# Kernel tuning notes

Hardware: AMD Instinct MI355X
Metric: run time of the kernel (lower is better)

The kernel has to match this reference:

```python
import jax, jax.numpy as jnp
import numpy as np

N, E = 40000, 640000
IN_DIM, EDGE_DIM, HID = 128, 64, 128


def setup_inputs() -> dict:
    key = jax.random.key(0)
    ks = jax.random.split(key, 10)
    x = jax.random.normal(ks[0], (N, IN_DIM), dtype=jnp.float32)
    edge_index = jax.random.randint(ks[1], (2, E), 0, N, dtype=jnp.int64)
    edge_attr = jax.random.normal(ks[2], (E, EDGE_DIM), dtype=jnp.float32)
    # learned params (xavier-ish scaling)
    Wh_w = jax.random.normal(ks[3], (EDGE_DIM, HID), dtype=jnp.float32) / np.sqrt(EDGE_DIM)
    Wh_b = jnp.zeros((HID,), dtype=jnp.float32)
    Wn_w = jax.random.normal(ks[4], (2 * IN_DIM, HID), dtype=jnp.float32) / np.sqrt(2 * IN_DIM)
    Wn_b = jnp.zeros((HID,), dtype=jnp.float32)
    w_e = jax.random.normal(ks[5], (HID, 1), dtype=jnp.float32) / np.sqrt(HID)
    ft_w = jax.random.normal(ks[6], (IN_DIM, IN_DIM), dtype=jnp.float32) / np.sqrt(IN_DIM)
    ft_b = jnp.zeros((IN_DIM,), dtype=jnp.float32)
    return {"x": x, "edge_index": edge_index, "edge_attr": edge_attr,
            "Wh_w": Wh_w, "Wh_b": Wh_b, "Wn_w": Wn_w, "Wn_b": Wn_b,
            "w_e": w_e, "ft_w": ft_w, "ft_b": ft_b}


def reference(x, edge_index, edge_attr, Wh_w, Wh_b, Wn_w, Wn_b, w_e, ft_w, ft_b):
    src, dst = edge_index[0], edge_index[1]
    # gather endpoint features and run edge MLP: relu(W_h(e) + W_n([x_src; x_dst]))
    node_feat = jnp.concatenate([x[src], x[dst]], axis=1)          # [E, 2*in_dim]
    edge_h = edge_attr @ Wh_w + Wh_b                               # [E, hid]
    node_h = node_feat @ Wn_w + Wn_b                               # [E, hid]
    combined = jax.nn.relu(edge_h + node_h)
    scores = (combined @ w_e)[:, 0]                                # [E]
    alpha = jax.nn.softmax(scores, axis=0)                         # softmax over all edges
    # scatter-add weighted dst features into src nodes (same-type branch)
    local = jnp.zeros_like(x).at[src].add(-alpha[:, None] * x[dst])
    out = x + local
    out = out + out @ ft_w + ft_b
    return out
```

## Files before the change

kernel.cpp:

```cpp
#include <hip/hip_runtime.h>
#include <math.h>

#define N_NODES 40000
#define E_EDGES 640000
#define IN_DIM 128
#define EDGE_DIM 64
#define HID 128
#define EB 10000
#define NPART (EB * 4)

typedef unsigned int u32;
typedef unsigned short u16;
typedef __attribute__((ext_vector_type(4))) float f32x4;
typedef __attribute__((ext_vector_type(8))) short bf16x8;

__device__ __forceinline__ float bf_lo(u32 d) { return __uint_as_float(d << 16); }
__device__ __forceinline__ float bf_hi(u32 d) { return __uint_as_float(d & 0xffff0000u); }
__device__ __forceinline__ u16 f2bf(float f) {
    u32 u = __float_as_uint(f);
    return (u16)((u + 0x7fffu + ((u >> 16) & 1u)) >> 16);
}
__device__ __forceinline__ u32 pack_bf(float lo, float hi) {
    return ((u32)f2bf(hi) << 16) | (u32)f2bf(lo);
}


__global__ __launch_bounds__(256) void k_init(const float* __restrict__ x,
                                              u16* __restrict__ xb,
                                              u32* __restrict__ counts) {
    int i = blockIdx.x * 256 + threadIdx.x;
    xb[i] = f2bf(x[i]);
    if (i < N_NODES) counts[i] = 0;
}

__global__ __launch_bounds__(256) void k_trans(const float* __restrict__ Whw,
                                               const float* __restrict__ Wnw,
                                               const float* __restrict__ ftw,
                                               u16* __restrict__ Whtb,
                                               u16* __restrict__ WnAT,
                                               u16* __restrict__ WnBT,
                                               u16* __restrict__ fttb) {
    int i = blockIdx.x * 256 + threadIdx.x;
    if (i < 8192) {
        int h = i >> 6, k = i & 63;
        Whtb[i] = f2bf(Whw[k * HID + h]);
    } else if (i < 24576) {
        int j = i - 8192, h = j >> 7, k = j & 127;
        WnAT[j] = f2bf(Wnw[k * HID + h]);
    } else if (i < 40960) {
        int j = i - 24576, h = j >> 7, k = j & 127;
        WnBT[j] = f2bf(Wnw[(IN_DIM + k) * HID + h]);
    } else {
        int j = i - 40960, h = j >> 7, k = j & 127;
        fttb[j] = f2bf(ftw[k * IN_DIM + h]);
    }
}

__global__ __launch_bounds__(256) void k_proj(const u16* __restrict__ xb,
                                              const u16* __restrict__ WnAT,
                                              const u16* __restrict__ WnBT,
                                              const float* __restrict__ Whb,
                                              const float* __restrict__ Wnb,
                                              u16* __restrict__ P1b,
                                              u16* __restrict__ P2b) {
    const int t = threadIdx.x, w = t >> 6, lane = t & 63;
    const int mrow = lane & 15, quad = lane >> 4;
    const int rowBase = blockIdx.x * 64 + w * 16;

    bf16x8 a[4];
    const u16* ar = xb + (size_t)(rowBase + mrow) * IN_DIM + quad * 8;
#pragma unroll
    for (int ks = 0; ks < 4; ++ks) a[ks] = *(const bf16x8*)(ar + ks * 32);

#pragma unroll
    for (int nt = 0; nt < 8; ++nt) {
        const u16* b1p = WnAT + (size_t)(nt * 16 + mrow) * IN_DIM + quad * 8;
        const u16* b2p = WnBT + (size_t)(nt * 16 + mrow) * IN_DIM + quad * 8;
        f32x4 c1 = {0.f, 0.f, 0.f, 0.f}, c2 = {0.f, 0.f, 0.f, 0.f};
#pragma unroll
        for (int ks = 0; ks < 4; ++ks) {
            c1 = __builtin_amdgcn_mfma_f32_16x16x32_bf16(a[ks], *(const bf16x8*)(b1p + ks * 32), c1, 0, 0, 0);
            c2 = __builtin_amdgcn_mfma_f32_16x16x32_bf16(a[ks], *(const bf16x8*)(b2p + ks * 32), c2, 0, 0, 0);
        }
        const int col = nt * 16 + mrow;
        const float bias = Whb[col] + Wnb[col];
#pragma unroll
        for (int r = 0; r < 4; ++r) {
            int row = rowBase + quad * 4 + r;
            P1b[(size_t)row * HID + col] = f2bf(c1[r] + bias);
            P2b[(size_t)row * HID + col] = f2bf(c2[r]);
        }
    }
}

__global__ __launch_bounds__(256) void k_hist(const int* __restrict__ eidx,
                                              u32* __restrict__ counts) {
    int e = blockIdx.x * 256 + threadIdx.x;
    atomicAdd(&counts[eidx[e]], 1u);
}

__global__ __launch_bounds__(1024) void k_scan(const u32* __restrict__ counts,
                                               u32* __restrict__ off,
                                               u32* __restrict__ cur) {
    __shared__ u32 sums[1024];
    const int t = threadIdx.x;
    const int CH = 40;
    u32 local[CH];
    u32 s = 0;
    const int base = t * CH;
#pragma unroll
    for (int i = 0; i < CH; ++i) {
        int idx = base + i;
        u32 c = (idx < N_NODES) ? counts[idx] : 0u;
        local[i] = s;
        s += c;
    }
    sums[t] = s;
    __syncthreads();
    for (int o = 1; o < 1024; o <<= 1) {
        u32 v = (t >= o) ? sums[t - o] : 0u;
        __syncthreads();
        sums[t] += v;
        __syncthreads();
    }
    const u32 pre = sums[t] - s;
#pragma unroll
    for (int i = 0; i < CH; ++i) {
        int idx = base + i;
        if (idx < N_NODES) {
            u32 v = pre + local[i];
            off[idx] = v;
            cur[idx] = v;
        }
    }
    if (t == 1023) off[N_NODES] = sums[1023];
}

__global__ __launch_bounds__(256) void k_edge(const int* __restrict__ eidx,
                                              const float* __restrict__ ea,
                                              const u16* __restrict__ Whtb,
                                              const u16* __restrict__ P1b,
                                              const u16* __restrict__ P2b,
                                              const float* __restrict__ we,
                                              u32* __restrict__ cur,
                                              uint2* __restrict__ sde,
                                              float* __restrict__ partials) {
    const int t = threadIdx.x, w = t >> 6, lane = t & 63;
    const int e0 = blockIdx.x * 64 + w * 16;
    const int mrow = lane & 15, quad = lane >> 4;

    const int srcm = eidx[e0 + mrow];
    const int dstm = eidx[E_EDGES + e0 + mrow];
    const u16* p1 = P1b + (size_t)srcm * HID + quad * 8;
    const u16* p2 = P2b + (size_t)dstm * HID + quad * 8;
    bf16x8 aP1[4], aP2[4];
#pragma unroll
    for (int ks = 0; ks < 4; ++ks) {
        aP1[ks] = *(const bf16x8*)(p1 + ks * 32);
        aP2[ks] = *(const bf16x8*)(p2 + ks * 32);
    }

    const float* arow = ea + (size_t)(e0 + mrow) * EDGE_DIM + quad * 8;
    float4 f0 = *(const float4*)(arow);
    float4 f1 = *(const float4*)(arow + 4);
    float4 f2 = *(const float4*)(arow + 32);
    float4 f3 = *(const float4*)(arow + 36);

    bf16x8 bIe, bIo;
    {
        const int hotj = mrow & 7;
        const bool ce = (quad == (mrow >> 3));
        const bool co = (quad == 2 + (mrow >> 3));
#pragma unroll
        for (int j = 0; j < 8; ++j) {
            bIe[j] = (short)((ce && j == hotj) ? 0x3F80 : 0);
            bIo[j] = (short)((co && j == hotj) ? 0x3F80 : 0);
        }
    }

    bf16x8 a0, a1;
    a0[0] = (short)f2bf(f0.x); a0[1] = (short)f2bf(f0.y);
    a0[2] = (short)f2bf(f0.z); a0[3] = (short)f2bf(f0.w);
    a0[4] = (short)f2bf(f1.x); a0[5] = (short)f2bf(f1.y);
    a0[6] = (short)f2bf(f1.z); a0[7] = (short)f2bf(f1.w);
    a1[0] = (short)f2bf(f2.x); a1[1] = (short)f2bf(f2.y);
    a1[2] = (short)f2bf(f2.z); a1[3] = (short)f2bf(f2.w);
    a1[4] = (short)f2bf(f3.x); a1[5] = (short)f2bf(f3.y);
    a1[6] = (short)f2bf(f3.z); a1[7] = (short)f2bf(f3.w);

    float wsum[4] = {0.f, 0.f, 0.f, 0.f};
    const u16* bbase = Whtb + (size_t)mrow * EDGE_DIM + quad * 8;
#pragma unroll
    for (int nt = 0; nt < 8; ++nt) {
        const u16* bp = bbase + nt * 16 * EDGE_DIM;
        bf16x8 b0 = *(const bf16x8*)(bp);
        bf16x8 b1 = *(const bf16x8*)(bp + 32);
        f32x4 c = {0.f, 0.f, 0.f, 0.f};
        c = __builtin_amdgcn_mfma_f32_16x16x32_bf16(a0, b0, c, 0, 0, 0);
        c = __builtin_amdgcn_mfma_f32_16x16x32_bf16(a1, b1, c, 0, 0, 0);
        const bf16x8 bI = (nt & 1) ? bIo : bIe;
        c = __builtin_amdgcn_mfma_f32_16x16x32_bf16(aP1[nt >> 1], bI, c, 0, 0, 0);
        c = __builtin_amdgcn_mfma_f32_16x16x32_bf16(aP2[nt >> 1], bI, c, 0, 0, 0);
        float wv = we[nt * 16 + mrow];
#pragma unroll
        for (int r = 0; r < 4; ++r)
            wsum[r] += fmaxf(c[r], 0.f) * wv;
    }

#pragma unroll
    for (int off = 1; off < 16; off <<= 1) {
#pragma unroll
        for (int r = 0; r < 4; ++r) wsum[r] += __shfl_xor(wsum[r], off, 16);
    }
    float ex[4]; float s4 = 0.f;
#pragma unroll
    for (int r = 0; r < 4; ++r) { ex[r] = __expf(wsum[r]); s4 += ex[r]; }

    u32 sArr[4], dArr[4];
#pragma unroll
    for (int r = 0; r < 4; ++r) {
        sArr[r] = (u32)__shfl(srcm, quad * 4 + r, 16);
        dArr[r] = (u32)__shfl(dstm, quad * 4 + r, 16);
    }

    if (mrow == 0) {
#pragma unroll
        for (int r = 0; r < 4; ++r) {
            u32 pos = atomicAdd(&cur[sArr[r]], 1u);
            sde[pos] = make_uint2(dArr[r], __float_as_uint(-ex[r]));
        }
    }

    s4 += __shfl_xor(s4, 16, 64);
    s4 += __shfl_xor(s4, 32, 64);
    if (lane == 0) partials[blockIdx.x * 4 + w] = s4;
}

__global__ __launch_bounds__(256) void k_sum(const float* __restrict__ partials,
                                             float* __restrict__ sumExp) {
    float s = 0.f;
    for (int i = threadIdx.x; i < NPART; i += 256) s += partials[i];
#pragma unroll
    for (int off = 1; off < 64; off <<= 1) s += __shfl_xor(s, off, 64);
    __shared__ float ws4[4];
    if ((threadIdx.x & 63) == 0) ws4[threadIdx.x >> 6] = s;
    __syncthreads();
    if (threadIdx.x == 0) sumExp[0] = ws4[0] + ws4[1] + ws4[2] + ws4[3];
}

__global__ __launch_bounds__(256) void k_accum(const u32* __restrict__ off,
                                               const uint2* __restrict__ sde,
                                               const float* __restrict__ sumExp,
                                               const u16* __restrict__ xb,
                                               float* __restrict__ out) {
    const float invS = 1.0f / sumExp[0];
    const int lane = threadIdx.x & 63;
    const int n = blockIdx.x * 4 + (threadIdx.x >> 6);
    const u32 o0 = off[n], o1 = off[n + 1];

    float acc0 = 0.f, acc1 = 0.f;
    for (u32 base = o0; base < o1; base += 64) {
        u32 j = base + (u32)lane;
        uint2 dv = make_uint2(0u, 0u);
        if (j < o1) dv = sde[j];
        int cnt = (int)min(64u, o1 - base);
        int jj = 0;
        for (; jj + 4 <= cnt; jj += 4) {
            u32 d0 = __shfl(dv.x, jj, 64),     d1 = __shfl(dv.x, jj + 1, 64);
            u32 d2 = __shfl(dv.x, jj + 2, 64), d3 = __shfl(dv.x, jj + 3, 64);
            float a0 = __uint_as_float(__shfl(dv.y, jj, 64));
            float a1 = __uint_as_float(__shfl(dv.y, jj + 1, 64));
            float a2 = __uint_as_float(__shfl(dv.y, jj + 2, 64));
            float a3 = __uint_as_float(__shfl(dv.y, jj + 3, 64));
            u32 q0 = ((const u32*)(xb + (size_t)d0 * IN_DIM))[lane];
            u32 q1 = ((const u32*)(xb + (size_t)d1 * IN_DIM))[lane];
            u32 q2 = ((const u32*)(xb + (size_t)d2 * IN_DIM))[lane];
            u32 q3 = ((const u32*)(xb + (size_t)d3 * IN_DIM))[lane];
            acc0 = fmaf(a0, bf_lo(q0), acc0); acc1 = fmaf(a0, bf_hi(q0), acc1);
            acc0 = fmaf(a1, bf_lo(q1), acc0); acc1 = fmaf(a1, bf_hi(q1), acc1);
            acc0 = fmaf(a2, bf_lo(q2), acc0); acc1 = fmaf(a2, bf_hi(q2), acc1);
            acc0 = fmaf(a3, bf_lo(q3), acc0); acc1 = fmaf(a3, bf_hi(q3), acc1);
        }
        for (; jj < cnt; ++jj) {
            u32 dst = __shfl(dv.x, jj, 64);
            float a = __uint_as_float(__shfl(dv.y, jj, 64));
            u32 q = ((const u32*)(xb + (size_t)dst * IN_DIM))[lane];
            acc0 = fmaf(a, bf_lo(q), acc0);
            acc1 = fmaf(a, bf_hi(q), acc1);
        }
    }
    float* op = out + (size_t)n * IN_DIM + 2 * lane;
    op[0] = acc0 * invS;
    op[1] = acc1 * invS;
}

__global__ __launch_bounds__(256) void k_final(const float* __restrict__ x,
                                               const u16* __restrict__ fttb,
                                               const float* __restrict__ ftb,
                                               float* __restrict__ out) {
    __shared__ u32 ybp[64][68];
    const int t = threadIdx.x;
    const int rb = blockIdx.x * 64;

    {
        const int rr = t >> 2, seg = t & 3;
        const float4* xp = (const float4*)(x + (size_t)(rb + rr) * IN_DIM + seg * 32);
        const float4* lp = (const float4*)(out + (size_t)(rb + rr) * IN_DIM + seg * 32);
#pragma unroll
        for (int i = 0; i < 4; ++i) {
            float4 xa = xp[2 * i], xc = xp[2 * i + 1];
            float4 la = lp[2 * i], lc = lp[2 * i + 1];
            uint4 o;
            o.x = pack_bf(xa.x + la.x, xa.y + la.y);
            o.y = pack_bf(xa.z + la.z, xa.w + la.w);
            o.z = pack_bf(xc.x + lc.x, xc.y + lc.y);
            o.w = pack_bf(xc.z + lc.z, xc.w + lc.w);
            *(uint4*)&ybp[rr][seg * 16 + i * 4] = o;
        }
    }
    __syncthreads();

    const int w = t >> 6, lane = t & 63;
    const int mrow = lane & 15, quad = lane >> 4;
    const int rowBase = rb + w * 16;

    bf16x8 a[4];
#pragma unroll
    for (int ks = 0; ks < 4; ++ks)
        a[ks] = *(const bf16x8*)&ybp[w * 16 + mrow][ks * 16 + quad * 4];

#pragma unroll
    for (int nt = 0; nt < 8; ++nt) {
        const u16* bp = fttb + (size_t)(nt * 16 + mrow) * IN_DIM + quad * 8;
        f32x4 c = {0.f, 0.f, 0.f, 0.f};
#pragma unroll
        for (int ks = 0; ks < 4; ++ks)
            c = __builtin_amdgcn_mfma_f32_16x16x32_bf16(a[ks], *(const bf16x8*)(bp + ks * 32), c, 0, 0, 0);
        const int col = nt * 16 + mrow;
        const float fb = ftb[col];
#pragma unroll
        for (int r = 0; r < 4; ++r) {
            int row = rowBase + quad * 4 + r;
            size_t idx = (size_t)row * IN_DIM + col;
            float y = x[idx] + out[idx];
            out[idx] = y + c[r] + fb;
        }
    }
}

extern "C" void kernel_launch(void* const* d_in, const int* in_sizes, int n_in,
                              void* d_out, int out_size, void* d_ws, size_t ws_size,
                              hipStream_t stream) {
    const float* x    = (const float*)d_in[0];
    const int*   eidx = (const int*)d_in[1];
    const float* ea   = (const float*)d_in[2];
    const float* Whw  = (const float*)d_in[3];
    const float* Whb  = (const float*)d_in[4];
    const float* Wnw  = (const float*)d_in[5];
    const float* Wnb  = (const float*)d_in[6];
    const float* we   = (const float*)d_in[7];
    const float* ftw  = (const float*)d_in[8];
    const float* ftb  = (const float*)d_in[9];
    float* out = (float*)d_out;

    uint2* sde      = (uint2*)d_ws;
    u16*   P1b      = (u16*)(sde + (size_t)E_EDGES);
    u16*   P2b      = P1b + (size_t)N_NODES * HID;
    u16*   xb       = P2b + (size_t)N_NODES * HID;
    u16*   Whtb     = xb + (size_t)N_NODES * IN_DIM;
    u16*   WnAT     = Whtb + (size_t)EDGE_DIM * HID;
    u16*   WnBT     = WnAT + (size_t)HID * IN_DIM;
    u16*   fttb     = WnBT + (size_t)HID * IN_DIM;
    float* partials = (float*)(fttb + (size_t)IN_DIM * IN_DIM);
    float* sumExp   = partials + NPART;
    u32*   counts   = (u32*)(sumExp + 1);
    u32*   off      = counts + N_NODES;
    u32*   cur      = off + N_NODES + 1;

    k_init <<<(N_NODES * IN_DIM) / 256, 256, 0, stream>>>(x, xb, counts);
    k_trans<<<224, 256, 0, stream>>>(Whw, Wnw, ftw, Whtb, WnAT, WnBT, fttb);
    k_proj <<<N_NODES / 64, 256, 0, stream>>>(xb, WnAT, WnBT, Whb, Wnb, P1b, P2b);
    k_hist <<<E_EDGES / 256, 256, 0, stream>>>(eidx, counts);
    k_scan <<<1, 1024, 0, stream>>>(counts, off, cur);
    k_edge <<<EB, 256, 0, stream>>>(eidx, ea, Whtb, P1b, P2b, we, cur, sde, partials);
    k_sum  <<<1, 256, 0, stream>>>(partials, sumExp);
    k_accum<<<N_NODES / 4, 256, 0, stream>>>(off, sde, sumExp, xb, out);
    k_final<<<N_NODES / 64, 256, 0, stream>>>(x, fttb, ftb, out);
}
```

Baseline: 577.1 us.

## Process edges in source-sorted order via a separate fill kernel

A new k_fill kernel does the counting-sort scatter, writing a permutation of (edge id, dst) into CSR positions. k_edge then walks edges in sorted order, gathering edge_attr and src indices through the permutation and writing sde contiguously instead of scattering with atomics. The aim is to remove the scattered atomics and writes from the MFMA-heavy edge kernel and to reuse P1 rows for consecutive edges that share a source. In exchange it adds a kernel launch, an extra pass over the edge indices, and random-access reads of the 256-byte edge_attr rows.

```diff
diff --git a/kernel.cpp b/kernel.cpp
--- a/kernel.cpp
+++ b/kernel.cpp
@@ -136,21 +136,34 @@
     if (t == 1023) off[N_NODES] = sums[1023];
 }
 
+__global__ __launch_bounds__(256) void k_fill(const int* __restrict__ eidx,
+                                              u32* __restrict__ cur,
+                                              uint2* __restrict__ perm2) {
+    int e = blockIdx.x * 256 + threadIdx.x;
+    int s = eidx[e];
+    int d = eidx[E_EDGES + e];
+    u32 pos = atomicAdd(&cur[s], 1u);
+    perm2[pos] = make_uint2((u32)e, (u32)d);
+}
+
 __global__ __launch_bounds__(256) void k_edge(const int* __restrict__ eidx,
                                               const float* __restrict__ ea,
                                               const u16* __restrict__ Whtb,
                                               const u16* __restrict__ P1b,
                                               const u16* __restrict__ P2b,
                                               const float* __restrict__ we,
-                                              u32* __restrict__ cur,
+                                              const uint2* __restrict__ perm2,
                                               uint2* __restrict__ sde,
                                               float* __restrict__ partials) {
     const int t = threadIdx.x, w = t >> 6, lane = t & 63;
-    const int e0 = blockIdx.x * 64 + w * 16;
+    const int j0 = blockIdx.x * 64 + w * 16;
     const int mrow = lane & 15, quad = lane >> 4;
 
-    const int srcm = eidx[e0 + mrow];
-    const int dstm = eidx[E_EDGES + e0 + mrow];
+    const uint2 pe = perm2[j0 + mrow];
+    const int em   = (int)pe.x;
+    const int dstm = (int)pe.y;
+    const int srcm = eidx[em];
+
     const u16* p1 = P1b + (size_t)srcm * HID + quad * 8;
     const u16* p2 = P2b + (size_t)dstm * HID + quad * 8;
     bf16x8 aP1[4], aP2[4];
@@ -160,7 +173,7 @@
         aP2[ks] = *(const bf16x8*)(p2 + ks * 32);
     }
 
-    const float* arow = ea + (size_t)(e0 + mrow) * EDGE_DIM + quad * 8;
+    const float* arow = ea + (size_t)em * EDGE_DIM + quad * 8;
     float4 f0 = *(const float4*)(arow);
     float4 f1 = *(const float4*)(arow + 4);
     float4 f2 = *(const float4*)(arow + 32);
@@ -216,19 +229,15 @@
 #pragma unroll
     for (int r = 0; r < 4; ++r) { ex[r] = __expf(wsum[r]); s4 += ex[r]; }
 
-    u32 sArr[4], dArr[4];
-#pragma unroll
-    for (int r = 0; r < 4; ++r) {
-        sArr[r] = (u32)__shfl(srcm, quad * 4 + r, 16);
+    u32 dArr[4];
+#pragma unroll
+    for (int r = 0; r < 4; ++r)
         dArr[r] = (u32)__shfl(dstm, quad * 4 + r, 16);
-    }
 
     if (mrow == 0) {
 #pragma unroll
-        for (int r = 0; r < 4; ++r) {
-            u32 pos = atomicAdd(&cur[sArr[r]], 1u);
-            sde[pos] = make_uint2(dArr[r], __float_as_uint(-ex[r]));
-        }
+        for (int r = 0; r < 4; ++r)
+            sde[j0 + quad * 4 + r] = make_uint2(dArr[r], __float_as_uint(-ex[r]));
     }
 
     s4 += __shfl_xor(s4, 16, 64);
@@ -376,13 +385,15 @@
     u32*   counts   = (u32*)(sumExp + 1);
     u32*   off      = counts + N_NODES;
     u32*   cur      = off + N_NODES + 1;
+    uint2* perm2    = (uint2*)(cur + N_NODES);
 
     k_init <<<(N_NODES * IN_DIM) / 256, 256, 0, stream>>>(x, xb, counts);
     k_trans<<<224, 256, 0, stream>>>(Whw, Wnw, ftw, Whtb, WnAT, WnBT, fttb);
     k_proj <<<N_NODES / 64, 256, 0, stream>>>(xb, WnAT, WnBT, Whb, Wnb, P1b, P2b);
     k_hist <<<E_EDGES / 256, 256, 0, stream>>>(eidx, counts);
     k_scan <<<1, 1024, 0, stream>>>(counts, off, cur);
-    k_edge <<<EB, 256, 0, stream>>>(eidx, ea, Whtb, P1b, P2b, we, cur, sde, partials);
+    k_fill <<<E_EDGES / 256, 256, 0, stream>>>(eidx, cur, perm2);
+    k_edge <<<EB, 256, 0, stream>>>(eidx, ea, Whtb, P1b, P2b, we, perm2, sde, partials);
     k_sum  <<<1, 256, 0, stream>>>(partials, sumExp);
     k_accum<<<N_NODES / 4, 256, 0, stream>>>(off, sde, sumExp, xb, out);
     k_final<<<N_NODES / 64, 256, 0, stream>>>(x, fttb, ftb, out);
```

After: 595.5 us. 3.2% more time.
